# Kernel tuning notes

Hardware: AMD Instinct MI355X
Metric: run time of the kernel (lower is better)

The kernel has to match this reference:

```python
import jax, jax.numpy as jnp
import numpy as np

HEAD_DIM = 128
N_Q_HEADS = 16
N_KV_HEADS = 8
ROPE_THETA = 10000.0


def setup_inputs() -> dict:
    key = jax.random.key(0)
    ks = jax.random.split(key, 5)
    B, S, D, Hq, Hkv = 2, 2048, 4096, 2048, 1024
    sc = 0.02
    hidden_states = jax.random.normal(ks[0], (B, S, D), dtype=jnp.float32)
    wq = jax.random.normal(ks[1], (Hq, D), dtype=jnp.float32) * sc
    wk = jax.random.normal(ks[2], (Hkv, D), dtype=jnp.float32) * sc
    wv = jax.random.normal(ks[3], (Hkv, D), dtype=jnp.float32) * sc
    wo = jax.random.normal(ks[4], (D, Hq), dtype=jnp.float32) * sc
    position_ids = jnp.broadcast_to(jnp.arange(S, dtype=jnp.int64)[None, :], (B, S))
    return {"hidden_states": hidden_states, "position_ids": position_ids,
            "wq": wq, "wk": wk, "wv": wv, "wo": wo}


def _rope_cos_sin(position_ids, dtype):
    # Llama rotary embedding: inv_freq over even dims, emb = cat(freqs, freqs)
    inv_freq = 1.0 / (ROPE_THETA ** (jnp.arange(0, HEAD_DIM, 2, dtype=jnp.float32) / HEAD_DIM))
    freqs = position_ids.astype(jnp.float32)[:, :, None] * inv_freq[None, None, :]  # [B,S,d/2]
    emb = jnp.concatenate([freqs, freqs], axis=-1)  # [B,S,d]
    return jnp.cos(emb).astype(dtype), jnp.sin(emb).astype(dtype)


def _rotate_half(x):
    x1, x2 = jnp.split(x, 2, axis=-1)
    return jnp.concatenate([-x2, x1], axis=-1)


def reference(hidden_states, position_ids, wq, wk, wv, wo):
    B, S, D = hidden_states.shape
    dh = HEAD_DIM
    q = (hidden_states @ wq.T).reshape(B, S, N_Q_HEADS, dh).transpose(0, 2, 1, 3)   # [B,Hq,S,d]
    k = (hidden_states @ wk.T).reshape(B, S, N_KV_HEADS, dh).transpose(0, 2, 1, 3)  # [B,Hkv,S,d]
    v = (hidden_states @ wv.T).reshape(B, S, N_KV_HEADS, dh).transpose(0, 2, 1, 3)

    cos, sin = _rope_cos_sin(position_ids, q.dtype)  # [B,S,d]
    cos, sin = cos[:, None, :, :], sin[:, None, :, :]
    q = q * cos + _rotate_half(q) * sin
    k = k * cos + _rotate_half(k) * sin

    # GQA repeat_interleave(groups, dim=1)
    groups = N_Q_HEADS // N_KV_HEADS
    k = jnp.repeat(k, groups, axis=1)  # [B,Hq,S,d]
    v = jnp.repeat(v, groups, axis=1)

    scale = 1.0 / jnp.sqrt(jnp.asarray(dh, dtype=q.dtype))
    scores = jnp.einsum('bhqd,bhkd->bhqk', q, k) * scale
    causal = jnp.tril(jnp.ones((S, S), dtype=bool))
    scores = jnp.where(causal[None, None, :, :], scores, jnp.finfo(scores.dtype).min)
    probs = jax.nn.softmax(scores, axis=-1)
    attn = jnp.einsum('bhqk,bhkd->bhqd', probs, v)  # [B,Hq,S,d]
    attn = attn.transpose(0, 2, 1, 3).reshape(B, S, N_Q_HEADS * dh)
    return attn @ wo.T
```

## Files before the change

### kernel.cpp

```cpp
#include <hip/hip_runtime.h>
#include <cstdint>
#include <cstddef>

#define B_ 2
#define S_ 2048
#define NQKV 4096
#define HQ 16
#define HKV 8
#define DH 128
#define KOFF 2048
#define VOFF 3072

typedef __attribute__((ext_vector_type(4))) float f32x4;
typedef __attribute__((ext_vector_type(8))) short bf16x8;
typedef __attribute__((ext_vector_type(4))) unsigned int u32x4;
typedef const __attribute__((address_space(1))) void* gas1;
typedef __attribute__((address_space(3))) void* las3;
typedef __attribute__((address_space(3))) char* l3p;

__device__ __forceinline__ ushort f2b(float f) {
  union { float f; unsigned u; } x; x.f = f;
  return (ushort)((x.u + 0x7FFFu + ((x.u >> 16) & 1u)) >> 16);
}
__device__ __forceinline__ float b2f(ushort u) {
  union { unsigned u; float f; } x; x.u = ((unsigned)u) << 16; return x.f;
}

__global__ void prep_cast_kernel(const float4* __restrict__ hs,
                                 const float* __restrict__ wq, const float* __restrict__ wk,
                                 const float* __restrict__ wv,
                                 ushort4* __restrict__ xb, ushort4* __restrict__ wcat) {
  int bid = blockIdx.x;
  if (bid < 16384) {
    int i = bid * 256 + threadIdx.x;
    float4 v = hs[i];
    xb[i] = make_ushort4(f2b(v.x), f2b(v.y), f2b(v.z), f2b(v.w));
  } else {
    int i = (bid - 16384) * 256 + threadIdx.x;
    int row = i >> 10, c4 = i & 1023;
    const float* src = (row < 2048) ? (wq + (size_t)row * 4096)
                     : (row < 3072) ? (wk + (size_t)(row - 2048) * 4096)
                                    : (wv + (size_t)(row - 3072) * 4096);
    float4 v = ((const float4*)src)[c4];
    wcat[i] = make_ushort4(f2b(v.x), f2b(v.y), f2b(v.z), f2b(v.w));
  }
}

__global__ void cast_f32_bf16_kernel(const float4* __restrict__ in, ushort4* __restrict__ out) {
  int i = blockIdx.x * 256 + threadIdx.x;
  float4 v = in[i];
  out[i] = make_ushort4(f2b(v.x), f2b(v.y), f2b(v.z), f2b(v.w));
}

#define DSR(dst, addr, off) asm volatile("ds_read_b128 %0, %1 offset:" #off : "=v"(dst) : "v"(addr) : "memory")
#define MFMA16(d, a, b) d = __builtin_amdgcn_mfma_f32_16x16x32_bf16(a, b, d, 0, 0, 0)

template<int OUT_BF16>
__launch_bounds__(512, 2)
__global__ void gemm256(const ushort* __restrict__ A, const ushort* __restrict__ Bm,
                        void* __restrict__ C, int M, int N, int K) {
  __shared__ __attribute__((aligned(16))) char lds[131072];
  const int tid = threadIdx.x;
  const int lane = tid & 63;
  const int w = tid >> 6;
  const int wm = w >> 2, wn = w & 3;
  const int lr = lane & 15, lg = lane >> 4;

  const int nwg = gridDim.x;
  const int cpx = nwg >> 3;
  const int wg = blockIdx.x;
  const int swz = (wg & 7) * cpx + (wg >> 3);
  const int NT = N >> 8;
  const int bm = swz / NT, bn = swz % NT;
  const int m0 = bm * 256, n0 = bn * 256;

  const ushort* Ab = A + (size_t)m0 * K;
  const ushort* Bb = Bm + (size_t)n0 * K;

  const int NKT = K >> 6;

  int srow[2], scol[2];
#pragma unroll
  for (int jj = 0; jj < 2; ++jj) {
    int lb = (jj * 512 + tid) * 16;
    int ls = lb ^ (((lb >> 7) & 7) << 4);
    srow[jj] = ls >> 7;
    scol[jj] = (ls & 127) >> 1;
  }
  const int ldsw = w * 1024;

  auto stage2 = [&](int t, int j) {
    t = (t < NKT - 1) ? t : (NKT - 1);
    const int slot = ((t & 1) << 16) + (j << 14);
    const ushort* src = (j == 1 || j == 2) ? Ab : Bb;
    const int h = (j >= 2) ? 128 : 0;
    const int k0 = t << 6;
#pragma unroll
    for (int jj = 0; jj < 2; ++jj) {
      const ushort* g = src + (size_t)(h + srow[jj]) * K + k0 + scol[jj];
      __builtin_amdgcn_global_load_lds((gas1)(const void*)g,
          (las3)(void*)(lds + slot + jj * 8192 + ldsw), 16, 0, 0);
    }
  };

  const unsigned lds0 = (unsigned)(size_t)(l3p)(void*)lds;
  const int swzc = (lr & 7) << 4;
  const int c0 = (lg * 16) ^ swzc;
  const int c1 = (64 + lg * 16) ^ swzc;
  const unsigned baseA = lds0 + 16384u + wm * 16384u + lr * 128u;
  const unsigned baseB = lds0 + ((wn >> 1) ? 49152u : 0u) + ((wn & 1) * 64 + lr) * 128u;

  f32x4 zero = {0.0f, 0.0f, 0.0f, 0.0f};
  f32x4 acc[8][4];
#pragma unroll
  for (int m = 0; m < 8; ++m)
#pragma unroll
    for (int n = 0; n < 4; ++n) acc[m][n] = zero;

  stage2(0, 0); stage2(0, 1); stage2(0, 2); stage2(0, 3);
  stage2(1, 0); stage2(1, 1);
  asm volatile("s_waitcnt vmcnt(4)" ::: "memory");
  __builtin_amdgcn_s_barrier();

  for (int kt = 0; kt < NKT; ++kt) {
    const unsigned bo = (unsigned)((kt & 1) << 16);
    const unsigned aak0 = baseA + c0 + bo, aak1 = baseA + c1 + bo;
    const unsigned bak0 = baseB + c0 + bo, bak1 = baseB + c1 + bo;

    bf16x8 a0[2][4], a1[2][4], bq[2][2], bq2[2][2];

    DSR(a0[0][0], aak0, 0);    DSR(a0[0][1], aak0, 2048);
    DSR(a0[0][2], aak0, 4096); DSR(a0[0][3], aak0, 6144);
    DSR(a0[1][0], aak1, 0);    DSR(a0[1][1], aak1, 2048);
    DSR(a0[1][2], aak1, 4096); DSR(a0[1][3], aak1, 6144);
    DSR(bq[0][0], bak0, 0);    DSR(bq[0][1], bak0, 2048);
    DSR(bq[1][0], bak1, 0);    DSR(bq[1][1], bak1, 2048);
    stage2(kt + 1, 2);
    asm volatile("s_waitcnt lgkmcnt(8)" ::: "memory");
    __builtin_amdgcn_s_barrier();
    asm volatile("s_waitcnt lgkmcnt(0)" ::: "memory");
    __builtin_amdgcn_sched_barrier(0);
    __builtin_amdgcn_s_setprio(1);
#pragma unroll
    for (int kk = 0; kk < 2; ++kk)
#pragma unroll
      for (int m = 0; m < 4; ++m) {
        MFMA16(acc[m][0], a0[kk][m], bq[kk][0]);
        MFMA16(acc[m][1], a0[kk][m], bq[kk][1]);
      }
    __builtin_amdgcn_s_setprio(0);
    __builtin_amdgcn_s_barrier();

    DSR(bq2[0][0], bak0, 4096); DSR(bq2[0][1], bak0, 6144);
    DSR(bq2[1][0], bak1, 4096); DSR(bq2[1][1], bak1, 6144);
    stage2(kt + 1, 3);
    __builtin_amdgcn_s_barrier();
    asm volatile("s_waitcnt lgkmcnt(0)" ::: "memory");
    __builtin_amdgcn_sched_barrier(0);
    __builtin_amdgcn_s_setprio(1);
#pragma unroll
    for (int kk = 0; kk < 2; ++kk)
#pragma unroll
      for (int m = 0; m < 4; ++m) {
        MFMA16(acc[m][2], a0[kk][m], bq2[kk][0]);
        MFMA16(acc[m][3], a0[kk][m], bq2[kk][1]);
      }
    __builtin_amdgcn_s_setprio(0);
    __builtin_amdgcn_s_barrier();

    DSR(a1[0][0], aak0, 8192);  DSR(a1[0][1], aak0, 10240);
    DSR(a1[0][2], aak0, 12288); DSR(a1[0][3], aak0, 14336);
    DSR(a1[1][0], aak1, 8192);  DSR(a1[1][1], aak1, 10240);
    DSR(a1[1][2], aak1, 12288); DSR(a1[1][3], aak1, 14336);
    stage2(kt + 2, 0);
    __builtin_amdgcn_s_barrier();
    asm volatile("s_waitcnt lgkmcnt(0)" ::: "memory");
    __builtin_amdgcn_sched_barrier(0);
    __builtin_amdgcn_s_setprio(1);
#pragma unroll
    for (int kk = 0; kk < 2; ++kk)
#pragma unroll
      for (int m = 0; m < 4; ++m) {
        MFMA16(acc[m + 4][0], a1[kk][m], bq[kk][0]);
        MFMA16(acc[m + 4][1], a1[kk][m], bq[kk][1]);
      }
    __builtin_amdgcn_s_setprio(0);
    __builtin_amdgcn_s_barrier();

    stage2(kt + 2, 1);
    __builtin_amdgcn_s_barrier();
    __builtin_amdgcn_s_setprio(1);
#pragma unroll
    for (int kk = 0; kk < 2; ++kk)
#pragma unroll
      for (int m = 0; m < 4; ++m) {
        MFMA16(acc[m + 4][2], a1[kk][m], bq2[kk][0]);
        MFMA16(acc[m + 4][3], a1[kk][m], bq2[kk][1]);
      }
    __builtin_amdgcn_s_setprio(0);
    asm volatile("s_waitcnt vmcnt(4)" ::: "memory");
    __builtin_amdgcn_s_barrier();
  }

  asm volatile("s_waitcnt vmcnt(0)" ::: "memory");

#pragma unroll
  for (int m = 0; m < 8; ++m) {
    const int row0 = m0 + wm * 128 + m * 16 + lg * 4;
#pragma unroll
    for (int n = 0; n < 4; ++n) {
      const int col = n0 + wn * 64 + n * 16 + lr;
#pragma unroll
      for (int r = 0; r < 4; ++r) {
        if (OUT_BF16) ((ushort*)C)[(size_t)(row0 + r) * N + col] = f2b(acc[m][n][r]);
        else          ((float*)C)[(size_t)(row0 + r) * N + col] = acc[m][n][r];
      }
    }
  }
}

__global__ void rope_tv_kernel(ushort* __restrict__ qkv, ushort* __restrict__ vt) {
  __shared__ ushort tile[32][33];
  int bid = blockIdx.x;
  int tid = threadIdx.x;
  if (bid < 24576) {
    int t = bid * 256 + tid;
    int row = t / 1536;
    int idx = t - row * 1536;
    int head = idx >> 6, d = idx & 63;
    int pos = row & (S_ - 1);
    int col = (head < HQ) ? (head * DH + d) : (KOFF + (head - HQ) * DH + d);
    size_t base = (size_t)row * NQKV + col;
    float x1 = b2f(qkv[base]);
    float x2 = b2f(qkv[base + 64]);
    float inv = exp2f((float)d * -0.2076205059304600f);
    float ang = (float)pos * inv;
    float c = cosf(ang), s = sinf(ang);
    qkv[base]      = f2b(x1 * c - x2 * s);
    qkv[base + 64] = f2b(x2 * c + x1 * s);
  } else {
    int b2 = bid - 24576;
    const int s0 = (b2 & 63) * 32, d0 = ((b2 >> 6) & 3) * 32;
    const int bh = b2 >> 8, b = bh >> 3, kvh = bh & 7;
    const int tx = tid & 31, ty = tid >> 5;
    const ushort* src = qkv + (size_t)(b * S_ + s0) * NQKV + VOFF + kvh * DH + d0;
#pragma unroll
    for (int j = 0; j < 32; j += 8)
      tile[ty + j][tx] = src[(size_t)(ty + j) * NQKV + tx];
    __syncthreads();
    ushort* dst = vt + (size_t)((b * HKV + kvh) * DH + d0) * S_ + s0;
#pragma unroll
    for (int j = 0; j < 32; j += 8)
      dst[(size_t)(ty + j) * S_ + tx] = tile[tx][ty + j];
  }
}

__launch_bounds__(256, 2)
__global__ void attn_kernel(const ushort* __restrict__ qkv, const ushort* __restrict__ vt,
                            ushort* __restrict__ aout) {
  __shared__ ushort Ks[64 * DH];
  __shared__ ushort Vts[DH * 64];
  __shared__ ushort Ps[4][16 * 64];
  __shared__ ushort Es[4][16 * 128];
  const int tid = threadIdx.x, lane = tid & 63, w = tid >> 6;
  const int wg = blockIdx.x;
  const int swz = (wg & 7) * 64 + (wg >> 3);
  const int bh = swz >> 4, qi0 = swz & 15;
  const int b = bh >> 4, h = bh & 15, kvh = h >> 1;
  const int lr = lane & 15, lg = lane >> 4;

  const ushort* Kp = qkv + (size_t)(b * S_) * NQKV + KOFF + kvh * DH;
  const ushort* Vtp = vt + (size_t)(b * HKV + kvh) * DH * S_;
  ushort* Psw = &Ps[w][0];

  int koff[4], kb[4], voff[4], vb[4];
#pragma unroll
  for (int i = 0; i < 4; ++i) {
    int chunk = i * 256 + tid;
    int krow = chunk >> 4, kc = (chunk & 15) * 8;
    koff[i] = krow * NQKV + kc;
    kb[i] = (krow * 256 + kc * 2) ^ ((krow & 7) << 4);
    int vrow = chunk >> 3, vc = (chunk & 7) * 8;
    voff[i] = vrow * S_ + vc;
    vb[i] = (vrow * 128 + vc * 2) ^ ((vrow & 7) << 4);
  }

  f32x4 zero = {0.0f, 0.0f, 0.0f, 0.0f};
  const float SCALE_LOG2E = 0.12751744116470802f;

  for (int pass = 0; pass < 2; ++pass) {
    const int qi = pass ? (31 - qi0) : qi0;
    const int qt0 = qi * 64;
    const int qrow = qt0 + w * 16;
    const int q_lane = qrow + lr;

    bf16x8 qf[4];
    {
      const ushort* Qp = qkv + (size_t)(b * S_ + qrow + lr) * NQKV + h * DH;
#pragma unroll
      for (int ds = 0; ds < 4; ++ds)
        qf[ds] = *(const bf16x8*)(Qp + ds * 32 + lg * 8);
    }

    float m_run = -1e30f, l_run = 0.0f;
    f32x4 acc_o[8];
#pragma unroll
    for (int n = 0; n < 8; ++n) acc_o[n] = zero;

    const int ntiles = qi + 1;
    u32x4 kreg[4], vreg[4];

#pragma unroll
    for (int i = 0; i < 4; ++i) {
      kreg[i] = *(const u32x4*)(Kp + koff[i]);
      vreg[i] = *(const u32x4*)(Vtp + voff[i]);
    }
    __syncthreads();
#pragma unroll
    for (int i = 0; i < 4; ++i) {
      *(u32x4*)((char*)Ks + kb[i]) = kreg[i];
      *(u32x4*)((char*)Vts + vb[i]) = vreg[i];
    }
    __syncthreads();

    for (int t = 0; t < ntiles; ++t) {
      const int kv0 = t * 64;
      if (t + 1 < ntiles) {
        const int kv1 = kv0 + 64;
#pragma unroll
        for (int i = 0; i < 4; ++i) {
          kreg[i] = *(const u32x4*)(Kp + (size_t)kv1 * NQKV + koff[i]);
          vreg[i] = *(const u32x4*)(Vtp + kv1 + voff[i]);
        }
      }

      f32x4 sacc[4];
      __builtin_amdgcn_s_setprio(1);
#pragma unroll
      for (int ct = 0; ct < 4; ++ct) {
        sacc[ct] = zero;
#pragma unroll
        for (int ds = 0; ds < 4; ++ds) {
          int krow = ct * 16 + lr;
          int kbb = (krow * 256 + (ds * 32 + lg * 8) * 2) ^ ((krow & 7) << 4);
          bf16x8 kf = *(const bf16x8*)((const char*)Ks + kbb);
          sacc[ct] = __builtin_amdgcn_mfma_f32_16x16x32_bf16(kf, qf[ds], sacc[ct], 0, 0, 0);
        }
      }
      __builtin_amdgcn_s_setprio(0);

      float sv[4][4];
      float mx = -1e30f;
#pragma unroll
      for (int ct = 0; ct < 4; ++ct)
#pragma unroll
        for (int r = 0; r < 4; ++r) {
          int kv = kv0 + ct * 16 + lg * 4 + r;
          float x = sacc[ct][r] * SCALE_LOG2E;
          sv[ct][r] = (kv <= q_lane) ? x : -1e30f;
          mx = fmaxf(mx, sv[ct][r]);
        }
      mx = fmaxf(mx, __shfl_xor(mx, 16, 64));
      mx = fmaxf(mx, __shfl_xor(mx, 32, 64));
      if (!__all(mx <= m_run + 8.0f)) {
        float mnew = fmaxf(m_run, mx);
        float alpha = __builtin_amdgcn_exp2f(m_run - mnew);
        l_run *= alpha;
#pragma unroll
        for (int n = 0; n < 8; ++n)
#pragma unroll
          for (int r = 0; r < 4; ++r) acc_o[n][r] *= alpha;
        m_run = mnew;
      }
      float psum = 0.0f;
#pragma unroll
      for (int ct = 0; ct < 4; ++ct)
#pragma unroll
        for (int r = 0; r < 4; ++r) {
          float p = __builtin_amdgcn_exp2f(sv[ct][r] - m_run);
          psum += p;
          int kvl = ct * 16 + lg * 4 + r;
          int pb = (lr * 128 + kvl * 2) ^ ((lr & 7) << 4);
          *(ushort*)((char*)Psw + pb) = f2b(p);
        }
      psum += __shfl_xor(psum, 16, 64);
      psum += __shfl_xor(psum, 32, 64);
      l_run += psum;

      asm volatile("s_waitcnt lgkmcnt(0)" ::: "memory");
      __builtin_amdgcn_sched_barrier(0);

      __builtin_amdgcn_s_setprio(1);
#pragma unroll
      for (int ks = 0; ks < 2; ++ks) {
        int pb = (lr * 128 + (ks * 32 + lg * 8) * 2) ^ ((lr & 7) << 4);
        bf16x8 pf = *(const bf16x8*)((const char*)Psw + pb);
#pragma unroll
        for (int n = 0; n < 8; ++n) {
          int vrow = n * 16 + lr;
          int vbb = (vrow * 128 + (ks * 32 + lg * 8) * 2) ^ ((vrow & 7) << 4);
          bf16x8 vf = *(const bf16x8*)((const char*)Vts + vbb);
          acc_o[n] = __builtin_amdgcn_mfma_f32_16x16x32_bf16(vf, pf, acc_o[n], 0, 0, 0);
        }
      }
      __builtin_amdgcn_s_setprio(0);

      if (t + 1 < ntiles) {
        __syncthreads();
#pragma unroll
        for (int i = 0; i < 4; ++i) {
          *(u32x4*)((char*)Ks + kb[i]) = kreg[i];
          *(u32x4*)((char*)Vts + vb[i]) = vreg[i];
        }
        __syncthreads();
      }
    }

    float rl = 1.0f / l_run;
    char* Ew = (char*)&Es[w][0];
#pragma unroll
    for (int n = 0; n < 8; ++n)
#pragma unroll
      for (int rp = 0; rp < 2; ++rp) {
        unsigned lo = f2b(acc_o[n][2 * rp] * rl);
        unsigned hi = f2b(acc_o[n][2 * rp + 1] * rl);
        int d = n * 16 + lg * 4 + 2 * rp;
        int eb = (lr * 256 + d * 2) ^ ((lr & 7) << 4);
        *(unsigned*)(Ew + eb) = lo | (hi << 16);
      }
    ushort* Ap = aout + (size_t)(b * S_ + qrow) * 2048 + h * DH;
#pragma unroll
    for (int it = 0; it < 4; ++it) {
      int c = it * 64 + lane;
      int q = c >> 4, k16 = c & 15;
      int rb = (q * 256 + k16 * 16) ^ ((q & 7) << 4);
      u32x4 v = *(const u32x4*)(Ew + rb);
      *(u32x4*)((char*)(Ap + (size_t)q * 2048) + k16 * 16) = v;
    }
  }
}

extern "C" void kernel_launch(void* const* d_in, const int* in_sizes, int n_in,
                              void* d_out, int out_size, void* d_ws, size_t ws_size,
                              hipStream_t stream) {
  const float* hs = (const float*)d_in[0];
  const float* wq = (const float*)d_in[2];
  const float* wk = (const float*)d_in[3];
  const float* wv = (const float*)d_in[4];
  const float* wo = (const float*)d_in[5];
  char* ws = (char*)d_ws;

  ushort* Xb   = (ushort*)(ws + 0);
  ushort* Wcat = (ushort*)(ws + 33554432);
  ushort* QKV  = (ushort*)(ws + 67108864);
  ushort* Vt   = (ushort*)(ws + 100663296);
  ushort* Wob  = Xb;
  ushort* Aout = Wcat;

  prep_cast_kernel<<<32768, 256, 0, stream>>>((const float4*)hs, wq, wk, wv,
                                              (ushort4*)Xb, (ushort4*)Wcat);
  gemm256<1><<<256, 512, 0, stream>>>(Xb, Wcat, QKV, 4096, 4096, 4096);
  rope_tv_kernel<<<28672, 256, 0, stream>>>(QKV, Vt);
  cast_f32_bf16_kernel<<<8192, 256, 0, stream>>>((const float4*)wo, (ushort4*)Wob);
  attn_kernel<<<dim3(512), 256, 0, stream>>>(QKV, Vt, Aout);
  gemm256<0><<<256, 512, 0, stream>>>(Aout, Wob, (float*)d_out, 4096, 4096, 2048);
}
```

Before: 308.0 us.

## Split KV tiles across wave pairs in attention and merge partial softmax states

The attention kernel now runs 8 waves per block, with each pair of waves sharing a 16-row query slice. Within a pair, the two waves process alternating 64-key tiles, which are loaded two at a time into double-sized K/V shared buffers. At the end, the odd wave writes its partial output and max/sum statistics to shared memory, and the even wave rescales and combines them before storing. The goal is more parallelism per query block and roughly half the serial KV-loop length per wave, at the cost of an extra merge step, more shared memory, and a clamped duplicate tile load when the tile count is odd.

```diff
diff --git a/kernel.cpp b/kernel.cpp
--- a/kernel.cpp
+++ b/kernel.cpp
@@ -255,14 +255,14 @@
   }
 }
 
-__launch_bounds__(256, 2)
+__launch_bounds__(512, 4)
 __global__ void attn_kernel(const ushort* __restrict__ qkv, const ushort* __restrict__ vt,
                             ushort* __restrict__ aout) {
-  __shared__ ushort Ks[64 * DH];
-  __shared__ ushort Vts[DH * 64];
-  __shared__ ushort Ps[4][16 * 64];
-  __shared__ ushort Es[4][16 * 128];
+  __shared__ ushort Ks[2][64 * DH];
+  __shared__ ushort Vts[2][DH * 64];
+  __shared__ ushort Ps[8][16 * 64];
   const int tid = threadIdx.x, lane = tid & 63, w = tid >> 6;
+  const int qsub = w >> 1, kvhalf = w & 1;
   const int wg = blockIdx.x;
   const int swz = (wg & 7) * 64 + (wg >> 3);
   const int bh = swz >> 4, qi0 = swz & 15;
@@ -272,17 +272,21 @@
   const ushort* Kp = qkv + (size_t)(b * S_) * NQKV + KOFF + kvh * DH;
   const ushort* Vtp = vt + (size_t)(b * HKV + kvh) * DH * S_;
   ushort* Psw = &Ps[w][0];
-
-  int koff[4], kb[4], voff[4], vb[4];
+  float* MLm = (float*)&Ps[0][0];
+  float* MLl = MLm + 512;
+
+  int koff[4], kb[4], voff[4], vb[4], tadd[4];
 #pragma unroll
   for (int i = 0; i < 4; ++i) {
-    int chunk = i * 256 + tid;
-    int krow = chunk >> 4, kc = (chunk & 15) * 8;
+    int c = i * 512 + tid;
+    int tp = c >> 10, cc = c & 1023;
+    tadd[i] = tp;
+    int krow = cc >> 4, kc = (cc & 15) * 8;
     koff[i] = krow * NQKV + kc;
-    kb[i] = (krow * 256 + kc * 2) ^ ((krow & 7) << 4);
-    int vrow = chunk >> 3, vc = (chunk & 7) * 8;
+    kb[i] = tp * 16384 + ((krow * 256 + kc * 2) ^ ((krow & 7) << 4));
+    int vrow = cc >> 3, vc = (cc & 7) * 8;
     voff[i] = vrow * S_ + vc;
-    vb[i] = (vrow * 128 + vc * 2) ^ ((vrow & 7) << 4);
+    vb[i] = tp * 16384 + ((vrow * 128 + vc * 2) ^ ((vrow & 7) << 4));
   }
 
   f32x4 zero = {0.0f, 0.0f, 0.0f, 0.0f};
@@ -291,8 +295,10 @@
   for (int pass = 0; pass < 2; ++pass) {
     const int qi = pass ? (31 - qi0) : qi0;
     const int qt0 = qi * 64;
-    const int qrow = qt0 + w * 16;
+    const int qrow = qt0 + qsub * 16;
     const int q_lane = qrow + lr;
+    const int ntiles = qi + 1;
+    const int npairs = (ntiles + 1) >> 1;
 
     bf16x8 qf[4];
     {
@@ -307,135 +313,163 @@
 #pragma unroll
     for (int n = 0; n < 8; ++n) acc_o[n] = zero;
 
-    const int ntiles = qi + 1;
     u32x4 kreg[4], vreg[4];
 
 #pragma unroll
     for (int i = 0; i < 4; ++i) {
-      kreg[i] = *(const u32x4*)(Kp + koff[i]);
-      vreg[i] = *(const u32x4*)(Vtp + voff[i]);
+      int tt = tadd[i]; tt = (tt < ntiles) ? tt : (ntiles - 1);
+      kreg[i] = *(const u32x4*)(Kp + (size_t)(tt * 64) * NQKV + koff[i]);
+      vreg[i] = *(const u32x4*)(Vtp + (size_t)voff[i] + tt * 64);
     }
     __syncthreads();
 #pragma unroll
     for (int i = 0; i < 4; ++i) {
-      *(u32x4*)((char*)Ks + kb[i]) = kreg[i];
-      *(u32x4*)((char*)Vts + vb[i]) = vreg[i];
+      *(u32x4*)((char*)&Ks[0][0] + kb[i]) = kreg[i];
+      *(u32x4*)((char*)&Vts[0][0] + vb[i]) = vreg[i];
     }
     __syncthreads();
 
-    for (int t = 0; t < ntiles; ++t) {
-      const int kv0 = t * 64;
-      if (t + 1 < ntiles) {
-        const int kv1 = kv0 + 64;
+    for (int j = 0; j < npairs; ++j) {
+      if (j + 1 < npairs) {
+        const int tb = 2 * j + 2;
 #pragma unroll
         for (int i = 0; i < 4; ++i) {
-          kreg[i] = *(const u32x4*)(Kp + (size_t)kv1 * NQKV + koff[i]);
-          vreg[i] = *(const u32x4*)(Vtp + kv1 + voff[i]);
+          int tt = tb + tadd[i]; tt = (tt < ntiles) ? tt : (ntiles - 1);
+          kreg[i] = *(const u32x4*)(Kp + (size_t)(tt * 64) * NQKV + koff[i]);
+          vreg[i] = *(const u32x4*)(Vtp + (size_t)voff[i] + tt * 64);
         }
       }
 
-      f32x4 sacc[4];
-      __builtin_amdgcn_s_setprio(1);
-#pragma unroll
-      for (int ct = 0; ct < 4; ++ct) {
-        sacc[ct] = zero;
-#pragma unroll
-        for (int ds = 0; ds < 4; ++ds) {
-          int krow = ct * 16 + lr;
-          int kbb = (krow * 256 + (ds * 32 + lg * 8) * 2) ^ ((krow & 7) << 4);
-          bf16x8 kf = *(const bf16x8*)((const char*)Ks + kbb);
-          sacc[ct] = __builtin_amdgcn_mfma_f32_16x16x32_bf16(kf, qf[ds], sacc[ct], 0, 0, 0);
+      const int t = 2 * j + kvhalf;
+      if (t < ntiles) {
+        const int kv0 = t * 64;
+        const char* Ksw = (const char*)&Ks[kvhalf][0];
+        const char* Vtsw = (const char*)&Vts[kvhalf][0];
+
+        f32x4 sacc[4];
+        __builtin_amdgcn_s_setprio(1);
+#pragma unroll
+        for (int ct = 0; ct < 4; ++ct) {
+          sacc[ct] = zero;
+#pragma unroll
+          for (int ds = 0; ds < 4; ++ds) {
+            int krow = ct * 16 + lr;
+            int kbb = (krow * 256 + (ds * 32 + lg * 8) * 2) ^ ((krow & 7) << 4);
+            bf16x8 kf = *(const bf16x8*)(Ksw + kbb);
+            sacc[ct] = __builtin_amdgcn_mfma_f32_16x16x32_bf16(kf, qf[ds], sacc[ct], 0, 0, 0);
+          }
         }
-      }
-      __builtin_amdgcn_s_setprio(0);
-
-      float sv[4][4];
-      float mx = -1e30f;
-#pragma unroll
-      for (int ct = 0; ct < 4; ++ct)
-#pragma unroll
-        for (int r = 0; r < 4; ++r) {
-          int kv = kv0 + ct * 16 + lg * 4 + r;
-          float x = sacc[ct][r] * SCALE_LOG2E;
-          sv[ct][r] = (kv <= q_lane) ? x : -1e30f;
-          mx = fmaxf(mx, sv[ct][r]);
+        __builtin_amdgcn_s_setprio(0);
+
+        float sv[4][4];
+        float mx = -1e30f;
+#pragma unroll
+        for (int ct = 0; ct < 4; ++ct)
+#pragma unroll
+          for (int r = 0; r < 4; ++r) {
+            int kv = kv0 + ct * 16 + lg * 4 + r;
+            float x = sacc[ct][r] * SCALE_LOG2E;
+            sv[ct][r] = (kv <= q_lane) ? x : -1e30f;
+            mx = fmaxf(mx, sv[ct][r]);
+          }
+        mx = fmaxf(mx, __shfl_xor(mx, 16, 64));
+        mx = fmaxf(mx, __shfl_xor(mx, 32, 64));
+        if (!__all(mx <= m_run + 8.0f)) {
+          float mnew = fmaxf(m_run, mx);
+          float alpha = __builtin_amdgcn_exp2f(m_run - mnew);
+          l_run *= alpha;
+#pragma unroll
+          for (int n = 0; n < 8; ++n)
+#pragma unroll
+            for (int r = 0; r < 4; ++r) acc_o[n][r] *= alpha;
+          m_run = mnew;
         }
-      mx = fmaxf(mx, __shfl_xor(mx, 16, 64));
-      mx = fmaxf(mx, __shfl_xor(mx, 32, 64));
-      if (!__all(mx <= m_run + 8.0f)) {
-        float mnew = fmaxf(m_run, mx);
-        float alpha = __builtin_amdgcn_exp2f(m_run - mnew);
-        l_run *= alpha;
-#pragma unroll
-        for (int n = 0; n < 8; ++n)
-#pragma unroll
-          for (int r = 0; r < 4; ++r) acc_o[n][r] *= alpha;
-        m_run = mnew;
-      }
-      float psum = 0.0f;
-#pragma unroll
-      for (int ct = 0; ct < 4; ++ct)
-#pragma unroll
-        for (int r = 0; r < 4; ++r) {
-          float p = __builtin_amdgcn_exp2f(sv[ct][r] - m_run);
-          psum += p;
-          int kvl = ct * 16 + lg * 4 + r;
-          int pb = (lr * 128 + kvl * 2) ^ ((lr & 7) << 4);
-          *(ushort*)((char*)Psw + pb) = f2b(p);
+        float psum = 0.0f;
+#pragma unroll
+        for (int ct = 0; ct < 4; ++ct)
+#pragma unroll
+          for (int r = 0; r < 4; ++r) {
+            float p = __builtin_amdgcn_exp2f(sv[ct][r] - m_run);
+            psum += p;
+            int kvl = ct * 16 + lg * 4 + r;
+            int pb = (lr * 128 + kvl * 2) ^ ((lr & 7) << 4);
+            *(ushort*)((char*)Psw + pb) = f2b(p);
+          }
+        psum += __shfl_xor(psum, 16, 64);
+        psum += __shfl_xor(psum, 32, 64);
+        l_run += psum;
+
+        asm volatile("s_waitcnt lgkmcnt(0)" ::: "memory");
+        __builtin_amdgcn_sched_barrier(0);
+
+        __builtin_amdgcn_s_setprio(1);
+#pragma unroll
+        for (int ks = 0; ks < 2; ++ks) {
+          int pb = (lr * 128 + (ks * 32 + lg * 8) * 2) ^ ((lr & 7) << 4);
+          bf16x8 pf = *(const bf16x8*)((const char*)Psw + pb);
+#pragma unroll
+          for (int n = 0; n < 8; ++n) {
+            int vrow = n * 16 + lr;
+            int vbb = (vrow * 128 + (ks * 32 + lg * 8) * 2) ^ ((vrow & 7) << 4);
+            bf16x8 vf = *(const bf16x8*)(Vtsw + vbb);
+            acc_o[n] = __builtin_amdgcn_mfma_f32_16x16x32_bf16(vf, pf, acc_o[n], 0, 0, 0);
+          }
         }
-      psum += __shfl_xor(psum, 16, 64);
-      psum += __shfl_xor(psum, 32, 64);
-      l_run += psum;
-
-      asm volatile("s_waitcnt lgkmcnt(0)" ::: "memory");
-      __builtin_amdgcn_sched_barrier(0);
-
-      __builtin_amdgcn_s_setprio(1);
-#pragma unroll
-      for (int ks = 0; ks < 2; ++ks) {
-        int pb = (lr * 128 + (ks * 32 + lg * 8) * 2) ^ ((lr & 7) << 4);
-        bf16x8 pf = *(const bf16x8*)((const char*)Psw + pb);
-#pragma unroll
-        for (int n = 0; n < 8; ++n) {
-          int vrow = n * 16 + lr;
-          int vbb = (vrow * 128 + (ks * 32 + lg * 8) * 2) ^ ((vrow & 7) << 4);
-          bf16x8 vf = *(const bf16x8*)((const char*)Vts + vbb);
-          acc_o[n] = __builtin_amdgcn_mfma_f32_16x16x32_bf16(vf, pf, acc_o[n], 0, 0, 0);
-        }
-      }
-      __builtin_amdgcn_s_setprio(0);
-
-      if (t + 1 < ntiles) {
+        __builtin_amdgcn_s_setprio(0);
+      }
+
+      if (j + 1 < npairs) {
         __syncthreads();
 #pragma unroll
         for (int i = 0; i < 4; ++i) {
-          *(u32x4*)((char*)Ks + kb[i]) = kreg[i];
-          *(u32x4*)((char*)Vts + vb[i]) = vreg[i];
+          *(u32x4*)((char*)&Ks[0][0] + kb[i]) = kreg[i];
+          *(u32x4*)((char*)&Vts[0][0] + vb[i]) = vreg[i];
         }
         __syncthreads();
       }
     }
 
-    float rl = 1.0f / l_run;
-    char* Ew = (char*)&Es[w][0];
-#pragma unroll
-    for (int n = 0; n < 8; ++n)
-#pragma unroll
-      for (int rp = 0; rp < 2; ++rp) {
-        unsigned lo = f2b(acc_o[n][2 * rp] * rl);
-        unsigned hi = f2b(acc_o[n][2 * rp + 1] * rl);
-        int d = n * 16 + lg * 4 + 2 * rp;
-        int eb = (lr * 256 + d * 2) ^ ((lr & 7) << 4);
-        *(unsigned*)(Ew + eb) = lo | (hi << 16);
-      }
-    ushort* Ap = aout + (size_t)(b * S_ + qrow) * 2048 + h * DH;
-#pragma unroll
-    for (int it = 0; it < 4; ++it) {
-      int c = it * 64 + lane;
-      int q = c >> 4, k16 = c & 15;
-      int rb = (q * 256 + k16 * 16) ^ ((q & 7) << 4);
-      u32x4 v = *(const u32x4*)(Ew + rb);
-      *(u32x4*)((char*)(Ap + (size_t)q * 2048) + k16 * 16) = v;
+    __syncthreads();
+    MLm[w * 64 + lane] = m_run;
+    MLl[w * 64 + lane] = l_run;
+    char* ox = (char*)&Vts[0][0] + qsub * 8192;
+    if (kvhalf == 1) {
+#pragma unroll
+      for (int n = 0; n < 8; ++n)
+        *(f32x4*)(ox + lane * 128 + ((n * 16) ^ ((lane & 7) << 4))) = acc_o[n];
+    }
+    __syncthreads();
+    if (kvhalf == 0) {
+      float pm = MLm[(w + 1) * 64 + lane];
+      float pl = MLl[(w + 1) * 64 + lane];
+      float mstar = fmaxf(m_run, pm);
+      float a0 = __builtin_amdgcn_exp2f(m_run - mstar);
+      float a1 = __builtin_amdgcn_exp2f(pm - mstar);
+      float lstar = l_run * a0 + pl * a1;
+      float rl = 1.0f / lstar;
+      char* Ew = (char*)&Ks[0][0] + qsub * 4096;
+#pragma unroll
+      for (int n = 0; n < 8; ++n) {
+        f32x4 po = *(const f32x4*)(ox + lane * 128 + ((n * 16) ^ ((lane & 7) << 4)));
+#pragma unroll
+        for (int rp = 0; rp < 2; ++rp) {
+          float v0 = (acc_o[n][2 * rp] * a0 + po[2 * rp] * a1) * rl;
+          float v1 = (acc_o[n][2 * rp + 1] * a0 + po[2 * rp + 1] * a1) * rl;
+          unsigned lo = f2b(v0), hi = f2b(v1);
+          int d = n * 16 + lg * 4 + 2 * rp;
+          int eb = (lr * 256 + d * 2) ^ ((lr & 7) << 4);
+          *(unsigned*)(Ew + eb) = lo | (hi << 16);
+        }
+      }
+      ushort* Ap = aout + (size_t)(b * S_ + qrow) * 2048 + h * DH;
+#pragma unroll
+      for (int it = 0; it < 4; ++it) {
+        int c = it * 64 + lane;
+        int q = c >> 4, k16 = c & 15;
+        int rb = (q * 256 + k16 * 16) ^ ((q & 7) << 4);
+        u32x4 v = *(const u32x4*)(Ew + rb);
+        *(u32x4*)((char*)(Ap + (size_t)q * 2048) + k16 * 16) = v;
+      }
     }
   }
 }
@@ -462,6 +496,6 @@
   gemm256<1><<<256, 512, 0, stream>>>(Xb, Wcat, QKV, 4096, 4096, 4096);
   rope_tv_kernel<<<28672, 256, 0, stream>>>(QKV, Vt);
   cast_f32_bf16_kernel<<<8192, 256, 0, stream>>>((const float4*)wo, (ushort4*)Wob);
-  attn_kernel<<<dim3(512), 256, 0, stream>>>(QKV, Vt, Aout);
+  attn_kernel<<<dim3(512), 512, 0, stream>>>(QKV, Vt, Aout);
   gemm256<0><<<256, 512, 0, stream>>>(Aout, Wob, (float*)d_out, 4096, 4096, 2048);
 }
```

Result: slower. 575.3 us (+86.8%).
